# Optimization experiments

Measured on AMD Instinct MI355X. Metric: run time of the kernel, lower is better.

## Reference

```python
import jax, jax.numpy as jnp
import numpy as np


def setup_inputs() -> dict:
    key = jax.random.key(0)
    ks = jax.random.split(key, 8)
    B, C, H, W = 32, 98, 128, 128
    F, D = 256, 128
    return {
        "hm": jax.random.normal(ks[0], (B, C, H, W), dtype=jnp.float32),
        "feat": jax.random.normal(ks[1], (B, F, H, W), dtype=jnp.float32),
        "W_embed": jax.random.normal(ks[2], (2 + 1 + F, D), dtype=jnp.float32) * 0.05,
        "b_embed": jax.random.normal(ks[3], (D,), dtype=jnp.float32) * 0.05,
        "A": jax.random.normal(ks[4], (C, C), dtype=jnp.float32) * 0.05,
        "W_gcn": jax.random.normal(ks[5], (D, D), dtype=jnp.float32) * 0.05,
        "W_out": jax.random.normal(ks[6], (D, 2), dtype=jnp.float32) * 0.05,
        "b_out": jax.random.normal(ks[7], (2,), dtype=jnp.float32) * 0.05,
    }


def reference(hm, feat, W_embed, b_embed, A, W_gcn, W_out, b_out):
    # hm: [B, C, H, W] per-landmark heatmaps; feat: [B, F, H, W] backbone features.
    B, C, H, W = hm.shape
    F = feat.shape[1]

    # decode_heatmap: per-(batch, landmark) argmax location over HxW (batched,
    # replacing the original per-sample Python loops).
    hm_flat = hm.reshape(B, C, H * W)
    idx = jnp.argmax(hm_flat, axis=-1)                      # [B, C] int
    ys = idx // W
    xs = idx % W

    # node confidences: hm[i, classIds, ys, xs] -> batched gather
    conf = jnp.take_along_axis(hm_flat, idx[:, :, None], axis=-1)[..., 0]  # [B, C]

    # pooling_feature: gather the F-dim feature vector at each landmark location
    feat_flat = feat.reshape(B, F, H * W)
    vis = jnp.take_along_axis(feat_flat, idx[:, None, :], axis=-1)  # [B, F, C]
    vis = jnp.transpose(vis, (0, 2, 1))                              # [B, C, F]

    # normalized positions: node_positions (x, y) / hm_size [h, w] (as in source)
    hm_size = jnp.array([H, W], dtype=hm.dtype)
    pos = jnp.stack([xs, ys], axis=-1).astype(hm.dtype) / hm_size    # [B, C, 2]

    # GCN over landmarks (batched instead of per-sample calls)
    node = jnp.concatenate([pos, conf[..., None], vis], axis=-1)     # [B, C, 2+1+F]
    h0 = jax.nn.relu(jnp.einsum("bcf,fd->bcd", node, W_embed) + b_embed)
    h1 = jax.nn.relu(jnp.einsum("ij,bjd,de->bie", A, h0, W_gcn))     # learned adjacency
    out = jnp.einsum("bcd,do->bco", h1, W_out) + b_out               # [B, C, 2]
    return hm, out
```

## Files before the change

### kernel.cpp

```cpp
#include <hip/hip_runtime.h>

#define HM_B 32
#define HM_C 98
#define HM_H 128
#define HM_W 128
#define HWSZ (HM_H * HM_W)
#define FDIM 256
#define DDIM 128
#define NODE_F (2 + 1 + FDIM)
#define NODE_P 260
#define BC (HM_B * HM_C)
#define HM_ELEMS ((size_t)BC * HWSZ)
#define LCHUNK 8
#define ICHUNK 7
#define NTHR 256

typedef float f32x4 __attribute__((ext_vector_type(4)));

__global__ __launch_bounds__(NTHR) void k1_copy_argmax_gather(
    const float* __restrict__ hm, const float* __restrict__ feat,
    float* __restrict__ out_hm, float* __restrict__ node_ws) {
    const int row = blockIdx.x;
    const int tid = threadIdx.x;
    const f32x4* __restrict__ src = (const f32x4*)(hm + (size_t)row * HWSZ);
    f32x4* __restrict__ dst = (f32x4*)(out_hm + (size_t)row * HWSZ);

    float bv = -INFINITY;
    int bi = 0;
    #pragma unroll
    for (int t = 0; t < HWSZ / 4 / NTHR; ++t) {
        const int p = t * NTHR + tid;
        const f32x4 v = __builtin_nontemporal_load(src + p);
        __builtin_nontemporal_store(v, dst + p);
        const float m4 = fmaxf(fmaxf(v[0], v[1]), fmaxf(v[2], v[3]));
        if (m4 > bv) {
            const int base = p * 4;
            if (v[0] > bv) { bv = v[0]; bi = base; }
            if (v[1] > bv) { bv = v[1]; bi = base + 1; }
            if (v[2] > bv) { bv = v[2]; bi = base + 2; }
            if (v[3] > bv) { bv = v[3]; bi = base + 3; }
        }
    }

    __shared__ float sv[NTHR];
    __shared__ int si[NTHR];
    sv[tid] = bv; si[tid] = bi;
    __syncthreads();
    for (int s = NTHR / 2; s > 0; s >>= 1) {
        if (tid < s) {
            const float ov = sv[tid + s];
            const int oi = si[tid + s];
            if (ov > sv[tid] || (ov == sv[tid] && oi < si[tid])) {
                sv[tid] = ov; si[tid] = oi;
            }
        }
        __syncthreads();
    }

    const int loc = si[0];
    const float conf = sv[0];
    const int b = row / HM_C;
    const float vis = feat[((size_t)(b * FDIM + tid)) * HWSZ + loc];
    float* nrow = node_ws + (size_t)row * NODE_P;
    nrow[3 + tid] = vis;
    if (tid == 0) {
        nrow[0] = (float)(loc % HM_W) * (1.0f / (float)HM_H);
        nrow[1] = (float)(loc / HM_W) * (1.0f / (float)HM_W);
        nrow[2] = conf;
    }
}

__global__ __launch_bounds__(NTHR) void k2_embed(
    float* __restrict__ node_ws, const float* __restrict__ W_embed,
    const float* __restrict__ b_embed) {
    const int bc0 = blockIdx.x * LCHUNK;
    const int tid = threadIdx.x;
    __shared__ float node_s[LCHUNK][NODE_P];

    #pragma unroll
    for (int l = 0; l < LCHUNK; ++l)
        for (int k = tid; k < NODE_F; k += NTHR)
            node_s[l][k] = node_ws[(size_t)(bc0 + l) * NODE_P + k];
    __syncthreads();

    const int d = tid & (DDIM - 1);
    const int lbase = (tid >> 7) * 4;
    const float bias = b_embed[d];
    float a0 = bias, a1 = bias, a2 = bias, a3 = bias;
    for (int f = 0; f < NODE_F; ++f) {
        const float w = W_embed[f * DDIM + d];
        a0 = fmaf(node_s[lbase + 0][f], w, a0);
        a1 = fmaf(node_s[lbase + 1][f], w, a1);
        a2 = fmaf(node_s[lbase + 2][f], w, a2);
        a3 = fmaf(node_s[lbase + 3][f], w, a3);
    }
    node_ws[(size_t)(bc0 + lbase + 0) * NODE_P + d] = fmaxf(a0, 0.f);
    node_ws[(size_t)(bc0 + lbase + 1) * NODE_P + d] = fmaxf(a1, 0.f);
    node_ws[(size_t)(bc0 + lbase + 2) * NODE_P + d] = fmaxf(a2, 0.f);
    node_ws[(size_t)(bc0 + lbase + 3) * NODE_P + d] = fmaxf(a3, 0.f);
}

__global__ __launch_bounds__(DDIM) void k3_gcn(
    const float* __restrict__ A, const float* __restrict__ node_ws,
    const float* __restrict__ W_gcn, const float* __restrict__ W_out,
    const float* __restrict__ b_out, float* __restrict__ out2) {
    const int b = blockIdx.x / (HM_C / ICHUNK);
    const int i0 = (blockIdx.x % (HM_C / ICHUNK)) * ICHUNK;
    const int tid = threadIdx.x;

    __shared__ float arow[ICHUNK * HM_C];
    __shared__ float tmp_s[ICHUNK * DDIM];
    __shared__ float h1_s[ICHUNK * DDIM];

    for (int k = tid; k < ICHUNK * HM_C; k += DDIM)
        arow[k] = A[(i0 + k / HM_C) * HM_C + (k % HM_C)];
    __syncthreads();

    {
        float acc[ICHUNK];
        #pragma unroll
        for (int i = 0; i < ICHUNK; ++i) acc[i] = 0.f;
        for (int j = 0; j < HM_C; ++j) {
            const float v = node_ws[((size_t)b * HM_C + j) * NODE_P + tid];
            #pragma unroll
            for (int i = 0; i < ICHUNK; ++i)
                acc[i] = fmaf(arow[i * HM_C + j], v, acc[i]);
        }
        #pragma unroll
        for (int i = 0; i < ICHUNK; ++i) tmp_s[i * DDIM + tid] = acc[i];
    }
    __syncthreads();

    {
        float acc[ICHUNK];
        #pragma unroll
        for (int i = 0; i < ICHUNK; ++i) acc[i] = 0.f;
        for (int k = 0; k < DDIM; ++k) {
            const float w = W_gcn[k * DDIM + tid];
            #pragma unroll
            for (int i = 0; i < ICHUNK; ++i)
                acc[i] = fmaf(tmp_s[i * DDIM + k], w, acc[i]);
        }
        #pragma unroll
        for (int i = 0; i < ICHUNK; ++i) h1_s[i * DDIM + tid] = fmaxf(acc[i], 0.f);
    }
    __syncthreads();

    if (tid < ICHUNK * 2) {
        const int i = tid >> 1;
        const int o = tid & 1;
        float acc = b_out[o];
        for (int dd = 0; dd < DDIM; ++dd)
            acc = fmaf(h1_s[i * DDIM + dd], W_out[dd * 2 + o], acc);
        out2[((size_t)b * HM_C + i0 + i) * 2 + o] = acc;
    }
}

extern "C" void kernel_launch(void* const* d_in, const int* in_sizes, int n_in,
                              void* d_out, int out_size, void* d_ws, size_t ws_size,
                              hipStream_t stream) {
    const float* hm      = (const float*)d_in[0];
    const float* feat    = (const float*)d_in[1];
    const float* W_embed = (const float*)d_in[2];
    const float* b_embed = (const float*)d_in[3];
    const float* A       = (const float*)d_in[4];
    const float* W_gcn   = (const float*)d_in[5];
    const float* W_out   = (const float*)d_in[6];
    const float* b_out   = (const float*)d_in[7];

    float* out_hm = (float*)d_out;
    float* out2   = (float*)d_out + HM_ELEMS;

    float* node_ws = (float*)d_ws;

    k1_copy_argmax_gather<<<BC, NTHR, 0, stream>>>(hm, feat, out_hm, node_ws);
    k2_embed<<<BC / LCHUNK, NTHR, 0, stream>>>(node_ws, W_embed, b_embed);
    k3_gcn<<<HM_B * (HM_C / ICHUNK), DDIM, 0, stream>>>(A, node_ws, W_gcn,
                                                        W_out, b_out, out2);
}
```

Baseline: 127.7 us.

## Split argmax rows across two blocks and move feature gather into embed kernel

Each heatmap row is now scanned by two blocks, each covering half the row, so there are twice as many blocks for the memory-bound copy+argmax pass. Partial results are merged in the embed kernel, which now also gathers the feature vectors. The block reduction uses wavefront shuffles instead of a shared-memory tree. Nontemporal load/store hints are dropped, and h0 is stored in a compact 128-wide buffer. The trade-off is an extra partial-result buffer and a scattered feature gather inside k2 that is no longer hidden behind the heatmap streaming.

Measured after the change: 135.4 us. +6.0%, slower.

```diff
diff --git a/kernel.cpp b/kernel.cpp
--- a/kernel.cpp
+++ b/kernel.cpp
@@ -5,6 +5,7 @@
 #define HM_H 128
 #define HM_W 128
 #define HWSZ (HM_H * HM_W)
+#define HALF (HWSZ / 2)
 #define FDIM 256
 #define DDIM 128
 #define NODE_F (2 + 1 + FDIM)
@@ -17,70 +18,81 @@
 
 typedef float f32x4 __attribute__((ext_vector_type(4)));
 
-__global__ __launch_bounds__(NTHR) void k1_copy_argmax_gather(
-    const float* __restrict__ hm, const float* __restrict__ feat,
-    float* __restrict__ out_hm, float* __restrict__ node_ws) {
-    const int row = blockIdx.x;
+__global__ __launch_bounds__(NTHR) void k1_copy_argmax(
+    const float* __restrict__ hm, float* __restrict__ out_hm,
+    float* __restrict__ pconf, int* __restrict__ pidx) {
+    const int bid = blockIdx.x;
+    const int row = bid >> 1;
+    const int half = bid & 1;
     const int tid = threadIdx.x;
-    const f32x4* __restrict__ src = (const f32x4*)(hm + (size_t)row * HWSZ);
-    f32x4* __restrict__ dst = (f32x4*)(out_hm + (size_t)row * HWSZ);
+    const size_t base = (size_t)row * HWSZ + (size_t)half * HALF;
+    const f32x4* __restrict__ src = (const f32x4*)(hm + base);
+    f32x4* __restrict__ dst = (f32x4*)(out_hm + base);
 
     float bv = -INFINITY;
     int bi = 0;
     #pragma unroll
-    for (int t = 0; t < HWSZ / 4 / NTHR; ++t) {
+    for (int t = 0; t < HALF / 4 / NTHR; ++t) {
         const int p = t * NTHR + tid;
-        const f32x4 v = __builtin_nontemporal_load(src + p);
-        __builtin_nontemporal_store(v, dst + p);
+        const f32x4 v = src[p];
+        dst[p] = v;
         const float m4 = fmaxf(fmaxf(v[0], v[1]), fmaxf(v[2], v[3]));
         if (m4 > bv) {
-            const int base = p * 4;
-            if (v[0] > bv) { bv = v[0]; bi = base; }
-            if (v[1] > bv) { bv = v[1]; bi = base + 1; }
-            if (v[2] > bv) { bv = v[2]; bi = base + 2; }
-            if (v[3] > bv) { bv = v[3]; bi = base + 3; }
+            const int gbase = half * HALF + p * 4;
+            if (v[0] > bv) { bv = v[0]; bi = gbase; }
+            if (v[1] > bv) { bv = v[1]; bi = gbase + 1; }
+            if (v[2] > bv) { bv = v[2]; bi = gbase + 2; }
+            if (v[3] > bv) { bv = v[3]; bi = gbase + 3; }
         }
     }
 
-    __shared__ float sv[NTHR];
-    __shared__ int si[NTHR];
-    sv[tid] = bv; si[tid] = bi;
-    __syncthreads();
-    for (int s = NTHR / 2; s > 0; s >>= 1) {
-        if (tid < s) {
-            const float ov = sv[tid + s];
-            const int oi = si[tid + s];
-            if (ov > sv[tid] || (ov == sv[tid] && oi < si[tid])) {
-                sv[tid] = ov; si[tid] = oi;
-            }
-        }
-        __syncthreads();
+    #pragma unroll
+    for (int s = 1; s < 64; s <<= 1) {
+        const float ov = __shfl_xor(bv, s, 64);
+        const int oi = __shfl_xor(bi, s, 64);
+        if (ov > bv || (ov == bv && oi < bi)) { bv = ov; bi = oi; }
     }
 
-    const int loc = si[0];
-    const float conf = sv[0];
-    const int b = row / HM_C;
-    const float vis = feat[((size_t)(b * FDIM + tid)) * HWSZ + loc];
-    float* nrow = node_ws + (size_t)row * NODE_P;
-    nrow[3 + tid] = vis;
+    __shared__ float wv[NTHR / 64];
+    __shared__ int wi[NTHR / 64];
+    if ((tid & 63) == 0) { wv[tid >> 6] = bv; wi[tid >> 6] = bi; }
+    __syncthreads();
     if (tid == 0) {
-        nrow[0] = (float)(loc % HM_W) * (1.0f / (float)HM_H);
-        nrow[1] = (float)(loc / HM_W) * (1.0f / (float)HM_W);
-        nrow[2] = conf;
+        float fv = wv[0]; int fi = wi[0];
+        #pragma unroll
+        for (int w = 1; w < NTHR / 64; ++w)
+            if (wv[w] > fv || (wv[w] == fv && wi[w] < fi)) { fv = wv[w]; fi = wi[w]; }
+        pconf[bid] = fv; pidx[bid] = fi;
     }
 }
 
 __global__ __launch_bounds__(NTHR) void k2_embed(
-    float* __restrict__ node_ws, const float* __restrict__ W_embed,
-    const float* __restrict__ b_embed) {
+    const float* __restrict__ feat, const float* __restrict__ pconf,
+    const int* __restrict__ pidx, const float* __restrict__ W_embed,
+    const float* __restrict__ b_embed, float* __restrict__ h0_ws) {
     const int bc0 = blockIdx.x * LCHUNK;
     const int tid = threadIdx.x;
     __shared__ float node_s[LCHUNK][NODE_P];
+    __shared__ int locs[LCHUNK];
+
+    if (tid < LCHUNK) {
+        const int row = bc0 + tid;
+        const float v0 = pconf[2 * row];
+        const float v1 = pconf[2 * row + 1];
+        const int loc = (v1 > v0) ? pidx[2 * row + 1] : pidx[2 * row];
+        locs[tid] = loc;
+        node_s[tid][0] = (float)(loc % HM_W) * (1.0f / (float)HM_H);
+        node_s[tid][1] = (float)(loc / HM_W) * (1.0f / (float)HM_W);
+        node_s[tid][2] = fmaxf(v0, v1);
+    }
+    __syncthreads();
 
     #pragma unroll
-    for (int l = 0; l < LCHUNK; ++l)
-        for (int k = tid; k < NODE_F; k += NTHR)
-            node_s[l][k] = node_ws[(size_t)(bc0 + l) * NODE_P + k];
+    for (int l = 0; l < LCHUNK; ++l) {
+        const int bcL = bc0 + l;
+        const int bb = bcL / HM_C;
+        node_s[l][3 + tid] = feat[((size_t)(bb * FDIM + tid)) * HWSZ + locs[l]];
+    }
     __syncthreads();
 
     const int d = tid & (DDIM - 1);
@@ -94,14 +106,14 @@
         a2 = fmaf(node_s[lbase + 2][f], w, a2);
         a3 = fmaf(node_s[lbase + 3][f], w, a3);
     }
-    node_ws[(size_t)(bc0 + lbase + 0) * NODE_P + d] = fmaxf(a0, 0.f);
-    node_ws[(size_t)(bc0 + lbase + 1) * NODE_P + d] = fmaxf(a1, 0.f);
-    node_ws[(size_t)(bc0 + lbase + 2) * NODE_P + d] = fmaxf(a2, 0.f);
-    node_ws[(size_t)(bc0 + lbase + 3) * NODE_P + d] = fmaxf(a3, 0.f);
+    h0_ws[(size_t)(bc0 + lbase + 0) * DDIM + d] = fmaxf(a0, 0.f);
+    h0_ws[(size_t)(bc0 + lbase + 1) * DDIM + d] = fmaxf(a1, 0.f);
+    h0_ws[(size_t)(bc0 + lbase + 2) * DDIM + d] = fmaxf(a2, 0.f);
+    h0_ws[(size_t)(bc0 + lbase + 3) * DDIM + d] = fmaxf(a3, 0.f);
 }
 
 __global__ __launch_bounds__(DDIM) void k3_gcn(
-    const float* __restrict__ A, const float* __restrict__ node_ws,
+    const float* __restrict__ A, const float* __restrict__ h0_ws,
     const float* __restrict__ W_gcn, const float* __restrict__ W_out,
     const float* __restrict__ b_out, float* __restrict__ out2) {
     const int b = blockIdx.x / (HM_C / ICHUNK);
@@ -121,7 +133,7 @@
         #pragma unroll
         for (int i = 0; i < ICHUNK; ++i) acc[i] = 0.f;
         for (int j = 0; j < HM_C; ++j) {
-            const float v = node_ws[((size_t)b * HM_C + j) * NODE_P + tid];
+            const float v = h0_ws[((size_t)b * HM_C + j) * DDIM + tid];
             #pragma unroll
             for (int i = 0; i < ICHUNK; ++i)
                 acc[i] = fmaf(arow[i * HM_C + j], v, acc[i]);
@@ -171,10 +183,14 @@
     float* out_hm = (float*)d_out;
     float* out2   = (float*)d_out + HM_ELEMS;
 
-    float* node_ws = (float*)d_ws;
+    char* ws = (char*)d_ws;
+    float* pconf = (float*)ws;  ws += 2 * BC * sizeof(float);
+    int*   pidx  = (int*)ws;    ws += 2 * BC * sizeof(int);
+    float* h0_ws = (float*)ws;
 
-    k1_copy_argmax_gather<<<BC, NTHR, 0, stream>>>(hm, feat, out_hm, node_ws);
-    k2_embed<<<BC / LCHUNK, NTHR, 0, stream>>>(node_ws, W_embed, b_embed);
-    k3_gcn<<<HM_B * (HM_C / ICHUNK), DDIM, 0, stream>>>(A, node_ws, W_gcn,
+    k1_copy_argmax<<<2 * BC, NTHR, 0, stream>>>(hm, out_hm, pconf, pidx);
+    k2_embed<<<BC / LCHUNK, NTHR, 0, stream>>>(feat, pconf, pidx,
+                                               W_embed, b_embed, h0_ws);
+    k3_gcn<<<HM_B * (HM_C / ICHUNK), DDIM, 0, stream>>>(A, h0_ws, W_gcn,
                                                         W_out, b_out, out2);
 }
```

## Fuse node embedding into argmax kernel and batch heatmap loads

Applied to the files above, without the earlier changes.

Merges the embedding matmul into the copy/argmax/gather kernel. Each block now builds its node vector in shared memory and computes the 128-dim embedding with a split-K across its two thread halves, which removes one launch and the node workspace round trip. The copy loop is also restructured to issue eight vector loads before consuming them, for more memory-level parallelism. The cost is that W_embed is re-read per row instead of per 8 rows, and the first kernel's tail gets longer.

After: 141.0 us. 1.1x slower.

```diff
diff --git a/kernel.cpp b/kernel.cpp
--- a/kernel.cpp
+++ b/kernel.cpp
@@ -8,18 +8,17 @@
 #define FDIM 256
 #define DDIM 128
 #define NODE_F (2 + 1 + FDIM)
-#define NODE_P 260
 #define BC (HM_B * HM_C)
 #define HM_ELEMS ((size_t)BC * HWSZ)
-#define LCHUNK 8
 #define ICHUNK 7
 #define NTHR 256
 
 typedef float f32x4 __attribute__((ext_vector_type(4)));
 
-__global__ __launch_bounds__(NTHR) void k1_copy_argmax_gather(
+__global__ __launch_bounds__(NTHR) void k1_fused(
     const float* __restrict__ hm, const float* __restrict__ feat,
-    float* __restrict__ out_hm, float* __restrict__ node_ws) {
+    const float* __restrict__ W_embed, const float* __restrict__ b_embed,
+    float* __restrict__ out_hm, float* __restrict__ h0_ws) {
     const int row = blockIdx.x;
     const int tid = threadIdx.x;
     const f32x4* __restrict__ src = (const f32x4*)(hm + (size_t)row * HWSZ);
@@ -28,22 +27,31 @@
     float bv = -INFINITY;
     int bi = 0;
     #pragma unroll
-    for (int t = 0; t < HWSZ / 4 / NTHR; ++t) {
-        const int p = t * NTHR + tid;
-        const f32x4 v = __builtin_nontemporal_load(src + p);
-        __builtin_nontemporal_store(v, dst + p);
-        const float m4 = fmaxf(fmaxf(v[0], v[1]), fmaxf(v[2], v[3]));
-        if (m4 > bv) {
-            const int base = p * 4;
-            if (v[0] > bv) { bv = v[0]; bi = base; }
-            if (v[1] > bv) { bv = v[1]; bi = base + 1; }
-            if (v[2] > bv) { bv = v[2]; bi = base + 2; }
-            if (v[3] > bv) { bv = v[3]; bi = base + 3; }
+    for (int g = 0; g < 2; ++g) {
+        f32x4 v[8];
+        #pragma unroll
+        for (int u = 0; u < 8; ++u)
+            v[u] = __builtin_nontemporal_load(src + (g * 8 + u) * NTHR + tid);
+        #pragma unroll
+        for (int u = 0; u < 8; ++u) {
+            const int p = (g * 8 + u) * NTHR + tid;
+            __builtin_nontemporal_store(v[u], dst + p);
+            const f32x4 x = v[u];
+            const float m4 = fmaxf(fmaxf(x[0], x[1]), fmaxf(x[2], x[3]));
+            if (m4 > bv) {
+                const int base = p * 4;
+                if (x[0] > bv) { bv = x[0]; bi = base; }
+                if (x[1] > bv) { bv = x[1]; bi = base + 1; }
+                if (x[2] > bv) { bv = x[2]; bi = base + 2; }
+                if (x[3] > bv) { bv = x[3]; bi = base + 3; }
+            }
         }
     }
 
     __shared__ float sv[NTHR];
     __shared__ int si[NTHR];
+    __shared__ float node_s[NODE_F + 1];
+    __shared__ float partial[NTHR];
     sv[tid] = bv; si[tid] = bi;
     __syncthreads();
     for (int s = NTHR / 2; s > 0; s >>= 1) {
@@ -58,50 +66,32 @@
     }
 
     const int loc = si[0];
-    const float conf = sv[0];
     const int b = row / HM_C;
-    const float vis = feat[((size_t)(b * FDIM + tid)) * HWSZ + loc];
-    float* nrow = node_ws + (size_t)row * NODE_P;
-    nrow[3 + tid] = vis;
+    node_s[3 + tid] = feat[((size_t)(b * FDIM + tid)) * HWSZ + loc];
     if (tid == 0) {
-        nrow[0] = (float)(loc % HM_W) * (1.0f / (float)HM_H);
-        nrow[1] = (float)(loc / HM_W) * (1.0f / (float)HM_W);
-        nrow[2] = conf;
+        node_s[0] = (float)(loc % HM_W) * (1.0f / (float)HM_H);
+        node_s[1] = (float)(loc / HM_W) * (1.0f / (float)HM_W);
+        node_s[2] = sv[0];
+    }
+    __syncthreads();
+
+    const int d = tid & (DDIM - 1);
+    const int h = tid >> 7;
+    const int f0 = h ? 130 : 0;
+    const int f1 = h ? NODE_F : 130;
+    float acc = 0.f;
+    for (int f = f0; f < f1; ++f)
+        acc = fmaf(node_s[f], W_embed[f * DDIM + d], acc);
+    partial[tid] = acc;
+    __syncthreads();
+    if (tid < DDIM) {
+        const float r = partial[tid] + partial[DDIM + tid] + b_embed[tid];
+        h0_ws[(size_t)row * DDIM + tid] = fmaxf(r, 0.f);
     }
 }
 
-__global__ __launch_bounds__(NTHR) void k2_embed(
-    float* __restrict__ node_ws, const float* __restrict__ W_embed,
-    const float* __restrict__ b_embed) {
-    const int bc0 = blockIdx.x * LCHUNK;
-    const int tid = threadIdx.x;
-    __shared__ float node_s[LCHUNK][NODE_P];
-
-    #pragma unroll
-    for (int l = 0; l < LCHUNK; ++l)
-        for (int k = tid; k < NODE_F; k += NTHR)
-            node_s[l][k] = node_ws[(size_t)(bc0 + l) * NODE_P + k];
-    __syncthreads();
-
-    const int d = tid & (DDIM - 1);
-    const int lbase = (tid >> 7) * 4;
-    const float bias = b_embed[d];
-    float a0 = bias, a1 = bias, a2 = bias, a3 = bias;
-    for (int f = 0; f < NODE_F; ++f) {
-        const float w = W_embed[f * DDIM + d];
-        a0 = fmaf(node_s[lbase + 0][f], w, a0);
-        a1 = fmaf(node_s[lbase + 1][f], w, a1);
-        a2 = fmaf(node_s[lbase + 2][f], w, a2);
-        a3 = fmaf(node_s[lbase + 3][f], w, a3);
-    }
-    node_ws[(size_t)(bc0 + lbase + 0) * NODE_P + d] = fmaxf(a0, 0.f);
-    node_ws[(size_t)(bc0 + lbase + 1) * NODE_P + d] = fmaxf(a1, 0.f);
-    node_ws[(size_t)(bc0 + lbase + 2) * NODE_P + d] = fmaxf(a2, 0.f);
-    node_ws[(size_t)(bc0 + lbase + 3) * NODE_P + d] = fmaxf(a3, 0.f);
-}
-
-__global__ __launch_bounds__(DDIM) void k3_gcn(
-    const float* __restrict__ A, const float* __restrict__ node_ws,
+__global__ __launch_bounds__(DDIM) void k2_gcn(
+    const float* __restrict__ A, const float* __restrict__ h0_ws,
     const float* __restrict__ W_gcn, const float* __restrict__ W_out,
     const float* __restrict__ b_out, float* __restrict__ out2) {
     const int b = blockIdx.x / (HM_C / ICHUNK);
@@ -121,7 +111,7 @@
         #pragma unroll
         for (int i = 0; i < ICHUNK; ++i) acc[i] = 0.f;
         for (int j = 0; j < HM_C; ++j) {
-            const float v = node_ws[((size_t)b * HM_C + j) * NODE_P + tid];
+            const float v = h0_ws[((size_t)b * HM_C + j) * DDIM + tid];
             #pragma unroll
             for (int i = 0; i < ICHUNK; ++i)
                 acc[i] = fmaf(arow[i * HM_C + j], v, acc[i]);
@@ -171,10 +161,9 @@
     float* out_hm = (float*)d_out;
     float* out2   = (float*)d_out + HM_ELEMS;
 
-    float* node_ws = (float*)d_ws;
+    float* h0_ws = (float*)d_ws;
 
-    k1_copy_argmax_gather<<<BC, NTHR, 0, stream>>>(hm, feat, out_hm, node_ws);
-    k2_embed<<<BC / LCHUNK, NTHR, 0, stream>>>(node_ws, W_embed, b_embed);
-    k3_gcn<<<HM_B * (HM_C / ICHUNK), DDIM, 0, stream>>>(A, node_ws, W_gcn,
+    k1_fused<<<BC, NTHR, 0, stream>>>(hm, feat, W_embed, b_embed, out_hm, h0_ws);
+    k2_gcn<<<HM_B * (HM_C / ICHUNK), DDIM, 0, stream>>>(A, h0_ws, W_gcn,
                                                         W_out, b_out, out2);
 }
```
